# Optimization experiments

Hardware: AMD Instinct MI355X
Metric: run time of the kernel (lower is better)

The kernel has to match this reference:

```python
import math
import jax, jax.numpy as jnp
import numpy as np

DIM = 1024
QK_DIM = 200
HIDDEN = 2 * DIM  # expansion_factor = 2
N = 8192


def setup_inputs() -> dict:
    key = jax.random.key(0)
    ks = jax.random.split(key, 8)
    s = 0.02
    return {
        "x": jax.random.normal(ks[0], (N, DIM), dtype=jnp.float32),
        "W_hidden": jax.random.normal(ks[1], (DIM, 2 * HIDDEN), dtype=jnp.float32) * s,
        "b_hidden": jnp.zeros((2 * HIDDEN,), dtype=jnp.float32),
        "W_qk": jax.random.normal(ks[2], (DIM, QK_DIM), dtype=jnp.float32) * s,
        "b_qk": jnp.zeros((QK_DIM,), dtype=jnp.float32),
        "gamma": 1.0 + jax.random.normal(ks[3], (2, QK_DIM), dtype=jnp.float32) * s,
        "beta": jnp.zeros((2, QK_DIM), dtype=jnp.float32),
        "W_out": jax.random.normal(ks[4], (HIDDEN, DIM), dtype=jnp.float32) * s,
        "b_out": jnp.zeros((DIM,), dtype=jnp.float32),
    }


def reference(x, W_hidden, b_hidden, W_qk, b_qk, gamma, beta, W_out, b_out):
    # to_hidden: Linear(dim -> 2*hidden) + SiLU, then chunk into v, gate
    hid = jax.nn.silu(x @ W_hidden + b_hidden)        # [N, 2H]
    v, gate = jnp.split(hid, 2, axis=-1)              # [N, H] each
    # to_qk: Linear(dim -> qk_dim) + SiLU
    qk = jax.nn.silu(x @ W_qk + b_qk)                 # [N, qk]
    # OffsetScale (heads=2): per-head affine on the shared qk
    q = qk * gamma[0] + beta[0]                       # [N, qk]
    k = qk * gamma[1] + beta[1]                       # [N, qk]
    # scores scaled by sqrt(dim) (module uses self.dim, not qk_dim)
    sim = (q @ k.T) * (1.0 / math.sqrt(x.shape[-1]))  # [N, N]
    # ReLU-squared attention (no softmax); dropout=0.0 -> identity
    attn = jnp.square(jax.nn.relu(sim))
    out = attn @ v                                    # [N, H]
    out = out * gate
    out = out @ W_out + b_out                         # [N, dim]
    # add_residual=True in this module multiplies by x
    return out * x
```

## Files before the change

kernel.cpp:

```cpp
#include <hip/hip_runtime.h>
#include <stdint.h>


typedef __bf16 bf16x8 __attribute__((ext_vector_type(8)));
typedef float f32x4 __attribute__((ext_vector_type(4)));

__device__ __forceinline__ uint16_t f2bf(float f) {
  uint32_t u = __builtin_bit_cast(uint32_t, f);
  u += 0x7fffu + ((u >> 16) & 1u);
  return (uint16_t)(u >> 16);
}
__device__ __forceinline__ float silu_f(float s) {
  return s / (1.f + __expf(-s));
}

__device__ __forceinline__ void gload16(const void* g, void* l) {
  __builtin_amdgcn_global_load_lds(
      (__attribute__((address_space(1))) void*)const_cast<void*>(g),
      (__attribute__((address_space(3))) void*)l, 16, 0, 0);
}


__global__ void cast_to_bf16(const float* __restrict__ in, uint16_t* __restrict__ out, int n4) {
  int i = blockIdx.x * blockDim.x + threadIdx.x;
  if (i < n4) {
    float4 f = ((const float4*)in)[i];
    ushort4 o;
    o.x = f2bf(f.x); o.y = f2bf(f.y); o.z = f2bf(f.z); o.w = f2bf(f.w);
    ((ushort4*)out)[i] = o;
  }
}

__global__ void transpose_cast_pad(const float* __restrict__ in, uint16_t* __restrict__ out,
                                   int R, int C, int Cp) {
  __shared__ float tile[32][33];
  int cb = blockIdx.x * 32;
  int rb = blockIdx.y * 32;
  int tx = threadIdx.x;
  int ty = threadIdx.y;
#pragma unroll
  for (int i = 0; i < 4; ++i) {
    int r = rb + ty + i * 8;
    int c = cb + tx;
    tile[ty + i * 8][tx] = (c < C) ? in[(size_t)r * C + c] : 0.f;
  }
  __syncthreads();
#pragma unroll
  for (int i = 0; i < 4; ++i) {
    int c = cb + ty + i * 8;
    if (c < Cp) out[(size_t)c * R + rb + tx] = f2bf(tile[tx][ty + i * 8]);
  }
}


struct EpiParams {
  const float* bias;
  const float* bias2;
  const float* g0;
  const float* b0;
  const float* g1;
  const float* b1;
  const uint16_t* gate;
  const float* x;
  uint16_t* o16a;
  uint16_t* o16b;
  uint16_t* oq;
  uint16_t* ok;
  float* o32;
};

__global__ __launch_bounds__(256) void k_hidqk(
    const uint16_t* __restrict__ A, const uint16_t* __restrict__ Bt, EpiParams p) {
  __shared__ __align__(16) uint16_t SH[128 * 64];
  uint16_t* As = SH;
  uint16_t* Bs = SH + 4096;

  const int tid = threadIdx.x;
  const int lane = tid & 63;
  const int wave = tid >> 6;
  const int wr = (wave >> 1) * 64;
  const int wc = (wave & 1) * 64;
  const int m0 = blockIdx.y * 128;
  const int n0 = blockIdx.x * 128;
  const int lda = 1024, ldb = 1024, K = 1024;

  f32x4 acc[4][4] = {};

  const int r0 = tid >> 2;
  const int q8 = (tid & 3) * 8;
  const uint16_t* gA0 = A + (size_t)(m0 + r0) * lda + q8;
  const uint16_t* gA1 = A + (size_t)(m0 + 64 + r0) * lda + q8;
  const uint16_t* gB0 = Bt + (size_t)(n0 + r0) * ldb + q8;
  const uint16_t* gB1 = Bt + (size_t)(n0 + 64 + r0) * ldb + q8;
  uint16_t* lA0 = As + wave * 512;
  uint16_t* lA1 = As + 2048 + wave * 512;
  uint16_t* lB0 = Bs + wave * 512;
  uint16_t* lB1 = Bs + 2048 + wave * 512;

  const int fr = lane & 15;
  const int rg = lane >> 4;
  const int kq = rg * 8;

  for (int k0 = 0; k0 < K; k0 += 32) {
    __syncthreads();
    gload16(gA0 + k0, lA0);
    gload16(gA1 + k0, lA1);
    gload16(gB0 + k0, lB0);
    gload16(gB1 + k0, lB1);
    __syncthreads();

    bf16x8 a[4], b[4];
#pragma unroll
    for (int i = 0; i < 4; ++i)
      a[i] = *(const bf16x8*)(As + (wr + i * 16 + fr) * 32 + kq);
#pragma unroll
    for (int j = 0; j < 4; ++j)
      b[j] = *(const bf16x8*)(Bs + (wc + j * 16 + fr) * 32 + kq);
#pragma unroll
    for (int i = 0; i < 4; ++i)
#pragma unroll
      for (int j = 0; j < 4; ++j)
        acc[i][j] = __builtin_amdgcn_mfma_f32_16x16x32_bf16(a[i], b[j], acc[i][j], 0, 0, 0);
  }

  if (n0 < 2048) {
    __syncthreads();
    uint16_t* ar = SH + wave * 2048;
    const int lrow = lane >> 3;
    const int mc = (lane & 7) * 8;
#pragma unroll
    for (int j = 0; j < 4; ++j) {
      const float bc = p.bias[n0 + wc + j * 16 + fr];
#pragma unroll
      for (int i = 0; i < 4; ++i)
#pragma unroll
        for (int r = 0; r < 4; ++r)
          ar[fr * 72 + i * 16 + rg * 4 + r] = f2bf(silu_f(acc[i][j][r] + bc));
#pragma unroll
      for (int rr = 0; rr < 2; ++rr) {
        bf16x8 v = *(const bf16x8*)(ar + (rr * 8 + lrow) * 72 + mc);
        *(bf16x8*)(p.o16a + (size_t)(n0 + wc + j * 16 + rr * 8 + lrow) * 8192 + m0 + wr + mc) = v;
      }
    }
  } else if (n0 < 4096) {
    __syncthreads();
    uint16_t* ar = SH + wave * 2048;
    const int lrow = lane >> 3;
    const int nc = (lane & 7) * 8;
    float bc[4];
#pragma unroll
    for (int j = 0; j < 4; ++j) bc[j] = p.bias[n0 + wc + j * 16 + fr];
#pragma unroll
    for (int i = 0; i < 4; ++i) {
#pragma unroll
      for (int j = 0; j < 4; ++j)
#pragma unroll
        for (int r = 0; r < 4; ++r)
          ar[(rg * 4 + r) * 72 + j * 16 + fr] = f2bf(silu_f(acc[i][j][r] + bc[j]));
#pragma unroll
      for (int rr = 0; rr < 2; ++rr) {
        bf16x8 v = *(const bf16x8*)(ar + (rr * 8 + lrow) * 72 + nc);
        *(bf16x8*)(p.o16b + (size_t)(m0 + wr + i * 16 + rr * 8 + lrow) * 2048 + (n0 - 2048) + wc + nc) = v;
      }
    }
  } else {
#pragma unroll
    for (int i = 0; i < 4; ++i) {
#pragma unroll
      for (int j = 0; j < 4; ++j) {
        const int row = m0 + wr + i * 16 + rg * 4;
        const int qc = n0 + wc + j * 16 + fr - 4096;
        if (qc < 224) {
#pragma unroll
          for (int r = 0; r < 4; ++r) {
            float qv = 0.f, kv = 0.f;
            if (qc < 200) {
              float s = silu_f(acc[i][j][r] + p.bias2[qc]);
              qv = s * p.g0[qc] + p.b0[qc];
              kv = s * p.g1[qc] + p.b1[qc];
            }
            p.oq[(size_t)(row + r) * 224 + qc] = f2bf(qv);
            p.ok[(size_t)(row + r) * 224 + qc] = f2bf(kv);
          }
        }
      }
    }
  }
}

__global__ __launch_bounds__(256) void k_attn(
    const uint16_t* __restrict__ Q,
    const uint16_t* __restrict__ Kt,
    uint16_t* __restrict__ attn) {
  __shared__ __align__(16) uint16_t As[128 * 32];
  __shared__ __align__(16) uint16_t Bs[128 * 32];
  __shared__ __align__(16) uint16_t Ep[4][2][16 * 72];

  const int tid = threadIdx.x;
  const int lane = tid & 63;
  const int wave = tid >> 6;
  const int wr = (wave >> 1) * 64;
  const int wc = (wave & 1) * 64;
  const int m0 = blockIdx.y * 128;
  const int n0 = blockIdx.x * 128;
  const int lda = 224, ldb = 224, K = 224;

  f32x4 acc[4][4] = {};

  const int r0 = tid >> 2;
  const int q8 = (tid & 3) * 8;
  const uint16_t* gA0 = Q + (size_t)(m0 + r0) * lda + q8;
  const uint16_t* gA1 = Q + (size_t)(m0 + 64 + r0) * lda + q8;
  const uint16_t* gB0 = Kt + (size_t)(n0 + r0) * ldb + q8;
  const uint16_t* gB1 = Kt + (size_t)(n0 + 64 + r0) * ldb + q8;
  uint16_t* lA0 = As + wave * 512;
  uint16_t* lA1 = As + 2048 + wave * 512;
  uint16_t* lB0 = Bs + wave * 512;
  uint16_t* lB1 = Bs + 2048 + wave * 512;

  const int fr = lane & 15;
  const int rg = lane >> 4;
  const int kq = rg * 8;

  for (int k0 = 0; k0 < K; k0 += 32) {
    __syncthreads();
    gload16(gA0 + k0, lA0);
    gload16(gA1 + k0, lA1);
    gload16(gB0 + k0, lB0);
    gload16(gB1 + k0, lB1);
    __syncthreads();

    bf16x8 a[4], b[4];
#pragma unroll
    for (int i = 0; i < 4; ++i)
      a[i] = *(const bf16x8*)(As + (wr + i * 16 + fr) * 32 + kq);
#pragma unroll
    for (int j = 0; j < 4; ++j)
      b[j] = *(const bf16x8*)(Bs + (wc + j * 16 + fr) * 32 + kq);
#pragma unroll
    for (int i = 0; i < 4; ++i)
#pragma unroll
      for (int j = 0; j < 4; ++j)
        acc[i][j] = __builtin_amdgcn_mfma_f32_16x16x32_bf16(a[i], b[j], acc[i][j], 0, 0, 0);
  }

#pragma unroll
  for (int i = 0; i < 4; ++i) {
    uint16_t* sl = Ep[wave][i & 1];
#pragma unroll
    for (int j = 0; j < 4; ++j)
#pragma unroll
      for (int r = 0; r < 4; ++r) {
        float s = fmaxf(acc[i][j][r] * 0.03125f, 0.f);
        sl[(rg * 4 + r) * 72 + j * 16 + fr] = f2bf(s * s);
      }
    const int row = lane >> 2;
    const int c0 = (lane & 3) * 16;
    bf16x8 v0 = *(const bf16x8*)(sl + row * 72 + c0);
    bf16x8 v1 = *(const bf16x8*)(sl + row * 72 + c0 + 8);
    uint16_t* dst = attn + (size_t)(m0 + wr + i * 16 + row) * 8192 + (n0 + wc + c0);
    *(bf16x8*)(dst) = v0;
    *(bf16x8*)(dst + 8) = v1;
  }
}

__global__ __launch_bounds__(512) void k_pv(
    const uint16_t* __restrict__ A, int lda,
    const uint16_t* __restrict__ Bt, int ldb,
    int K, int nx, EpiParams p) {
  __shared__ __align__(16) uint16_t SH[(128 + 256) * 32];
  uint16_t* As = SH;
  uint16_t* Bs = SH + 4096;

  const int id = blockIdx.x;
  const int bx = (id >> 3) % nx;
  const int by = (id & 7) + 8 * (id / (8 * nx));
  const int m0 = by * 128;
  const int n0 = bx * 256;

  const int tid = threadIdx.x;
  const int lane = tid & 63;
  const int wave = tid >> 6;
  const int wr = (wave & 1) * 64;
  const int wc = (wave >> 1) * 64;

  f32x4 acc[4][4] = {};

  const int r0 = tid >> 2;
  const int q8 = (tid & 3) * 8;
  const uint16_t* gA  = A  + (size_t)(m0 + r0) * lda + q8;
  const uint16_t* gB0 = Bt + (size_t)(n0 + r0) * ldb + q8;
  const uint16_t* gB1 = Bt + (size_t)(n0 + 128 + r0) * ldb + q8;
  uint16_t* lA  = As + wave * 512;
  uint16_t* lB0 = Bs + wave * 512;
  uint16_t* lB1 = Bs + 4096 + wave * 512;

  const int fr = lane & 15;
  const int rg = lane >> 4;
  const int kq = rg * 8;

  for (int k0 = 0; k0 < K; k0 += 32) {
    __syncthreads();
    gload16(gA + k0, lA);
    gload16(gB0 + k0, lB0);
    gload16(gB1 + k0, lB1);
    __syncthreads();

    bf16x8 a[4], b[4];
#pragma unroll
    for (int i = 0; i < 4; ++i)
      a[i] = *(const bf16x8*)(As + (wr + i * 16 + fr) * 32 + kq);
#pragma unroll
    for (int j = 0; j < 4; ++j)
      b[j] = *(const bf16x8*)(Bs + (wc + j * 16 + fr) * 32 + kq);
#pragma unroll
    for (int i = 0; i < 4; ++i)
#pragma unroll
      for (int j = 0; j < 4; ++j)
        acc[i][j] = __builtin_amdgcn_mfma_f32_16x16x32_bf16(a[i], b[j], acc[i][j], 0, 0, 0);
  }

  __syncthreads();
  uint16_t* ar = SH + wave * 1536;
  const int lrow = lane >> 3;
  const int nc = (lane & 7) * 8;
#pragma unroll
  for (int i = 0; i < 4; ++i) {
#pragma unroll
    for (int j = 0; j < 4; ++j)
#pragma unroll
      for (int r = 0; r < 4; ++r)
        ar[(rg * 4 + r) * 72 + j * 16 + fr] = f2bf(acc[i][j][r]);
#pragma unroll
    for (int rr = 0; rr < 2; ++rr) {
      const size_t base = (size_t)(m0 + wr + i * 16 + rr * 8 + lrow) * 2048 + n0 + wc + nc;
      bf16x8 v = *(const bf16x8*)(ar + (rr * 8 + lrow) * 72 + nc);
      bf16x8 g = *(const bf16x8*)(p.gate + base);
      bf16x8 o;
#pragma unroll
      for (int e = 0; e < 8; ++e) o[e] = (__bf16)((float)v[e] * (float)g[e]);
      *(bf16x8*)(p.o16a + base) = o;
    }
  }
}

__global__ __launch_bounds__(256) void k_final(
    const uint16_t* __restrict__ A,
    const uint16_t* __restrict__ Bt, EpiParams p) {
  __shared__ __align__(16) uint16_t As[128 * 32];
  __shared__ __align__(16) uint16_t Bs[128 * 32];

  const int tid = threadIdx.x;
  const int lane = tid & 63;
  const int wave = tid >> 6;
  const int wr = (wave >> 1) * 64;
  const int wc = (wave & 1) * 64;
  const int m0 = blockIdx.y * 128;
  const int n0 = blockIdx.x * 128;
  const int lda = 2048, ldb = 2048, K = 2048;

  f32x4 acc[4][4] = {};

  const int r0 = tid >> 2;
  const int q8 = (tid & 3) * 8;
  const uint16_t* gA0 = A + (size_t)(m0 + r0) * lda + q8;
  const uint16_t* gA1 = A + (size_t)(m0 + 64 + r0) * lda + q8;
  const uint16_t* gB0 = Bt + (size_t)(n0 + r0) * ldb + q8;
  const uint16_t* gB1 = Bt + (size_t)(n0 + 64 + r0) * ldb + q8;
  uint16_t* lA0 = As + wave * 512;
  uint16_t* lA1 = As + 2048 + wave * 512;
  uint16_t* lB0 = Bs + wave * 512;
  uint16_t* lB1 = Bs + 2048 + wave * 512;

  const int fr = lane & 15;
  const int kq = (lane >> 4) * 8;

  for (int k0 = 0; k0 < K; k0 += 32) {
    __syncthreads();
    gload16(gA0 + k0, lA0);
    gload16(gA1 + k0, lA1);
    gload16(gB0 + k0, lB0);
    gload16(gB1 + k0, lB1);
    __syncthreads();

    bf16x8 a[4], b[4];
#pragma unroll
    for (int i = 0; i < 4; ++i)
      a[i] = *(const bf16x8*)(As + (wr + i * 16 + fr) * 32 + kq);
#pragma unroll
    for (int j = 0; j < 4; ++j)
      b[j] = *(const bf16x8*)(Bs + (wc + j * 16 + fr) * 32 + kq);
#pragma unroll
    for (int i = 0; i < 4; ++i)
#pragma unroll
      for (int j = 0; j < 4; ++j)
        acc[i][j] = __builtin_amdgcn_mfma_f32_16x16x32_bf16(a[i], b[j], acc[i][j], 0, 0, 0);
  }

#pragma unroll
  for (int i = 0; i < 4; ++i) {
#pragma unroll
    for (int j = 0; j < 4; ++j) {
      const int row = m0 + wr + i * 16 + (lane >> 4) * 4;
      const int col = n0 + wc + j * 16 + fr;
      const float bc = p.bias[col];
#pragma unroll
      for (int r = 0; r < 4; ++r) {
        size_t idx = (size_t)(row + r) * 1024 + col;
        p.o32[idx] = (acc[i][j][r] + bc) * p.x[idx];
      }
    }
  }
}


extern "C" void kernel_launch(void* const* d_in, const int* in_sizes, int n_in,
                              void* d_out, int out_size, void* d_ws, size_t ws_size,
                              hipStream_t stream) {
  const float* x        = (const float*)d_in[0];
  const float* W_hidden = (const float*)d_in[1];
  const float* b_hidden = (const float*)d_in[2];
  const float* W_qk     = (const float*)d_in[3];
  const float* b_qk     = (const float*)d_in[4];
  const float* gamma    = (const float*)d_in[5];
  const float* beta     = (const float*)d_in[6];
  const float* W_out    = (const float*)d_in[7];
  const float* b_out    = (const float*)d_in[8];
  float* out = (float*)d_out;

  const bool fullM = ws_size >= (236ull << 20);
  const size_t region0 = fullM ? (128ull << 20) : (64ull << 20);

  char* base = (char*)d_ws;
  uint16_t* xb    = (uint16_t*)(base);
  uint16_t* WhT   = (uint16_t*)(base + (16ull << 20));
  uint16_t* WqkT  = (uint16_t*)(base + (24ull << 20));
  uint16_t* attnB = (uint16_t*)(base);
  char* tail = base + region0;
  uint16_t* WoT   = (uint16_t*)(tail);
  uint16_t* q     = (uint16_t*)(tail + (4ull << 20));
  uint16_t* kk    = (uint16_t*)(tail + (8ull << 20));
  uint16_t* vT    = (uint16_t*)(tail + (12ull << 20));
  uint16_t* gate  = (uint16_t*)(tail + (44ull << 20));
  uint16_t* out2g = (uint16_t*)(tail + (76ull << 20));
  (void)in_sizes; (void)n_in; (void)out_size;

  cast_to_bf16<<<(8192 * 1024 / 4) / 256, 256, 0, stream>>>(x, xb, 8192 * 1024 / 4);
  transpose_cast_pad<<<dim3(4096 / 32, 1024 / 32), dim3(32, 8), 0, stream>>>(W_hidden, WhT, 1024, 4096, 4096);
  transpose_cast_pad<<<dim3(256 / 32, 1024 / 32), dim3(32, 8), 0, stream>>>(W_qk, WqkT, 1024, 200, 256);
  transpose_cast_pad<<<dim3(1024 / 32, 2048 / 32), dim3(32, 8), 0, stream>>>(W_out, WoT, 2048, 1024, 1024);

  {
    EpiParams p{};
    p.bias = b_hidden; p.bias2 = b_qk;
    p.g0 = gamma; p.b0 = beta; p.g1 = gamma + 200; p.b1 = beta + 200;
    p.o16a = vT; p.o16b = gate; p.oq = q; p.ok = kk;
    k_hidqk<<<dim3(34, 64), 256, 0, stream>>>(xb, WhT, p);
  }

  if (fullM) {
    k_attn<<<dim3(64, 64), 256, 0, stream>>>(q, kk, attnB);
    {
      EpiParams p{};
      p.gate = gate; p.o16a = out2g;
      k_pv<<<dim3(8 * 64), 512, 0, stream>>>(attnB, 8192, vT, 8192, 8192, 8, p);
    }
  } else {
    for (int s = 0; s < 2; ++s) {
      k_attn<<<dim3(64, 32), 256, 0, stream>>>(q + (size_t)s * 4096 * 224, kk, attnB);
      {
        EpiParams p{};
        p.gate = gate + (size_t)s * 4096 * 2048;
        p.o16a = out2g + (size_t)s * 4096 * 2048;
        k_pv<<<dim3(8 * 32), 512, 0, stream>>>(attnB, 8192, vT, 8192, 8192, 8, p);
      }
    }
  }

  {
    EpiParams p{};
    p.bias = b_out; p.x = x; p.o32 = out;
    k_final<<<dim3(8, 64), 256, 0, stream>>>(out2g, WoT, p);
  }
}
```

Measured before the change: 636.0 us.

## Rewrite PV GEMM with 256x256 tiles, 4-stage LDS pipeline and swizzle

The attn@V kernel moves from 128x256 to 256x256 output tiles per block, doubling accumulators per wave. Global-to-LDS loads now run through a 4-buffer ring that prefetches three k-steps ahead, with split barriers, setprio around the MFMA bursts, and an XOR swizzle on LDS rows to cut bank conflicts. The goal is to hide memory latency behind MFMA work and raise operand reuse per loaded byte. The cost is a 128KB LDS footprint and heavy register use, and the grid halves to 256 blocks, which may leave CUs underfilled.

```diff
diff --git a/kernel.cpp b/kernel.cpp
--- a/kernel.cpp
+++ b/kernel.cpp
@@ -264,68 +264,109 @@
   }
 }
 
-__global__ __launch_bounds__(512) void k_pv(
+__global__ __launch_bounds__(512, 2) void k_pv(
     const uint16_t* __restrict__ A, int lda,
     const uint16_t* __restrict__ Bt, int ldb,
     int K, int nx, EpiParams p) {
-  __shared__ __align__(16) uint16_t SH[(128 + 256) * 32];
-  uint16_t* As = SH;
-  uint16_t* Bs = SH + 4096;
+  __shared__ __align__(16) uint16_t SH[65536];
 
   const int id = blockIdx.x;
   const int bx = (id >> 3) % nx;
   const int by = (id & 7) + 8 * (id / (8 * nx));
-  const int m0 = by * 128;
+  const int m0 = by * 256;
   const int n0 = bx * 256;
 
   const int tid = threadIdx.x;
   const int lane = tid & 63;
   const int wave = tid >> 6;
-  const int wr = (wave & 1) * 64;
-  const int wc = (wave >> 1) * 64;
-
-  f32x4 acc[4][4] = {};
-
-  const int r0 = tid >> 2;
-  const int q8 = (tid & 3) * 8;
-  const uint16_t* gA  = A  + (size_t)(m0 + r0) * lda + q8;
-  const uint16_t* gB0 = Bt + (size_t)(n0 + r0) * ldb + q8;
-  const uint16_t* gB1 = Bt + (size_t)(n0 + 128 + r0) * ldb + q8;
-  uint16_t* lA  = As + wave * 512;
-  uint16_t* lB0 = Bs + wave * 512;
-  uint16_t* lB1 = Bs + 4096 + wave * 512;
+  const int wrM = (wave >> 2) * 128;
+  const int wcN = (wave & 3) * 64;
 
   const int fr = lane & 15;
   const int rg = lane >> 4;
-  const int kq = rg * 8;
-
-  for (int k0 = 0; k0 < K; k0 += 32) {
-    __syncthreads();
-    gload16(gA + k0, lA);
-    gload16(gB0 + k0, lB0);
-    gload16(gB1 + k0, lB1);
-    __syncthreads();
-
-    bf16x8 a[4], b[4];
-#pragma unroll
-    for (int i = 0; i < 4; ++i)
-      a[i] = *(const bf16x8*)(As + (wr + i * 16 + fr) * 32 + kq);
-#pragma unroll
-    for (int j = 0; j < 4; ++j)
-      b[j] = *(const bf16x8*)(Bs + (wc + j * 16 + fr) * 32 + kq);
-#pragma unroll
-    for (int i = 0; i < 4; ++i)
-#pragma unroll
-      for (int j = 0; j < 4; ++j)
-        acc[i][j] = __builtin_amdgcn_mfma_f32_16x16x32_bf16(a[i], b[j], acc[i][j], 0, 0, 0);
-  }
-
-  __syncthreads();
-  uint16_t* ar = SH + wave * 1536;
+  const int swz = (rg ^ ((fr >> 1) & 3)) * 8;
+
+  const int rdA = (wrM + fr) * 32 + swz;
+  const int rdB = 8192 + (wcN + fr) * 32 + swz;
+
+  const int srow = lane >> 2;
+  const int sk = ((lane & 3) ^ ((lane >> 3) & 3)) * 8;
+  const uint16_t* gA0 = A + (size_t)(m0 + wave * 16 + srow) * lda + sk;
+  const uint16_t* gA1 = gA0 + (size_t)128 * lda;
+  const uint16_t* gB0 = Bt + (size_t)(n0 + wave * 16 + srow) * ldb + sk;
+  const uint16_t* gB1 = gB0 + (size_t)128 * ldb;
+
+  f32x4 acc[8][4] = {};
+  const int NT = K >> 5;
+
+  for (int s = 0; s < 3; ++s) {
+    const int ko = s * 32;
+    uint16_t* d = SH + s * 16384 + wave * 512;
+    gload16(gA0 + ko, d);
+    gload16(gA1 + ko, d + 4096);
+    gload16(gB0 + ko, d + 8192);
+    gload16(gB1 + ko, d + 12288);
+  }
+  asm volatile("s_waitcnt vmcnt(8)" ::: "memory");
+  __builtin_amdgcn_sched_barrier(0);
+  __builtin_amdgcn_s_barrier();
+  __builtin_amdgcn_sched_barrier(0);
+
+#define PV_TILE(T_, B_, BS_)                                                   \
+  do {                                                                         \
+    const uint16_t* bA_ = SH + (B_) * 16384;                                   \
+    const int kp_ = (((T_) + 3) & (NT - 1)) * 32;                              \
+    uint16_t* sd_ = SH + (BS_) * 16384 + wave * 512;                           \
+    bf16x8 aq[4], bq[4];                                                       \
+    _Pragma("unroll") for (int j = 0; j < 4; ++j)                              \
+        bq[j] = *(const bf16x8*)(bA_ + rdB + j * 512);                         \
+    _Pragma("unroll") for (int i = 0; i < 4; ++i)                              \
+        aq[i] = *(const bf16x8*)(bA_ + rdA + i * 512);                         \
+    gload16(gA0 + kp_, sd_);                                                   \
+    gload16(gA1 + kp_, sd_ + 4096);                                            \
+    __builtin_amdgcn_s_setprio(1);                                             \
+    _Pragma("unroll") for (int i = 0; i < 4; ++i)                              \
+      _Pragma("unroll") for (int j = 0; j < 4; ++j)                            \
+          acc[i][j] = __builtin_amdgcn_mfma_f32_16x16x32_bf16(                 \
+              aq[i], bq[j], acc[i][j], 0, 0, 0);                               \
+    __builtin_amdgcn_s_setprio(0);                                             \
+    __builtin_amdgcn_sched_barrier(0);                                         \
+    __builtin_amdgcn_s_barrier();                                              \
+    __builtin_amdgcn_sched_barrier(0);                                         \
+    _Pragma("unroll") for (int i = 0; i < 4; ++i)                              \
+        aq[i] = *(const bf16x8*)(bA_ + rdA + (4 + i) * 512);                   \
+    gload16(gB0 + kp_, sd_ + 8192);                                            \
+    gload16(gB1 + kp_, sd_ + 12288);                                           \
+    __builtin_amdgcn_s_setprio(1);                                             \
+    _Pragma("unroll") for (int i = 0; i < 4; ++i)                              \
+      _Pragma("unroll") for (int j = 0; j < 4; ++j)                            \
+          acc[4 + i][j] = __builtin_amdgcn_mfma_f32_16x16x32_bf16(             \
+              aq[i], bq[j], acc[4 + i][j], 0, 0, 0);                           \
+    __builtin_amdgcn_s_setprio(0);                                             \
+    asm volatile("s_waitcnt vmcnt(8)" ::: "memory");                           \
+    __builtin_amdgcn_sched_barrier(0);                                         \
+    __builtin_amdgcn_s_barrier();                                              \
+    __builtin_amdgcn_sched_barrier(0);                                         \
+  } while (0)
+
+  for (int t0 = 0; t0 < NT; t0 += 4) {
+    PV_TILE(t0 + 0, 0, 3);
+    PV_TILE(t0 + 1, 1, 0);
+    PV_TILE(t0 + 2, 2, 1);
+    PV_TILE(t0 + 3, 3, 2);
+  }
+#undef PV_TILE
+
+  asm volatile("s_waitcnt vmcnt(0)" ::: "memory");
+  __builtin_amdgcn_sched_barrier(0);
+  __builtin_amdgcn_s_barrier();
+  __builtin_amdgcn_sched_barrier(0);
+
+  uint16_t* ar = SH + wave * 2048;
   const int lrow = lane >> 3;
   const int nc = (lane & 7) * 8;
 #pragma unroll
-  for (int i = 0; i < 4; ++i) {
+  for (int i = 0; i < 8; ++i) {
 #pragma unroll
     for (int j = 0; j < 4; ++j)
 #pragma unroll
@@ -333,7 +374,7 @@
         ar[(rg * 4 + r) * 72 + j * 16 + fr] = f2bf(acc[i][j][r]);
 #pragma unroll
     for (int rr = 0; rr < 2; ++rr) {
-      const size_t base = (size_t)(m0 + wr + i * 16 + rr * 8 + lrow) * 2048 + n0 + wc + nc;
+      const size_t base = (size_t)(m0 + wrM + i * 16 + rr * 8 + lrow) * 2048 + n0 + wcN + nc;
       bf16x8 v = *(const bf16x8*)(ar + (rr * 8 + lrow) * 72 + nc);
       bf16x8 g = *(const bf16x8*)(p.gate + base);
       bf16x8 o;
@@ -463,7 +504,7 @@
     {
       EpiParams p{};
       p.gate = gate; p.o16a = out2g;
-      k_pv<<<dim3(8 * 64), 512, 0, stream>>>(attnB, 8192, vT, 8192, 8192, 8, p);
+      k_pv<<<dim3(8 * 32), 512, 0, stream>>>(attnB, 8192, vT, 8192, 8192, 8, p);
     }
   } else {
     for (int s = 0; s < 2; ++s) {
@@ -472,7 +513,7 @@
         EpiParams p{};
         p.gate = gate + (size_t)s * 4096 * 2048;
         p.o16a = out2g + (size_t)s * 4096 * 2048;
-        k_pv<<<dim3(8 * 32), 512, 0, stream>>>(attnB, 8192, vT, 8192, 8192, 8, p);
+        k_pv<<<dim3(8 * 16), 512, 0, stream>>>(attnB, 8192, vT, 8192, 8192, 8, p);
       }
     }
   }
```

After: 598.7 us. 1.06x faster.
